# Kernel tuning notes

Hardware: AMD Instinct MI355X
Metric: run time of the kernel (lower is better)

Reference implementation:

```python
import jax, jax.numpy as jnp
import numpy as np

EMB = 512
GP = 128
NH = 8
HD = EMB // NH  # 64
B = 2
S = 1024


def _rel_shift(x):
    # Faithful port of DoubleAttentionLayer._rel_shift (pads dim 1, reinterprets
    # (B, J+1, K, n) as (J+1, B, K, n), drops first slice). Row-major reshape
    # semantics match torch .view on contiguous tensors exactly.
    Bsz, J, K, N = x.shape
    zp = jnp.zeros((Bsz, 1, K, N), x.dtype)
    xp = jnp.concatenate([zp, x], axis=1).reshape(J + 1, Bsz, K, N)
    return xp[1:].reshape(Bsz, J, K, N)


def _layernorm(x):
    # nn.LayerNorm(emb_dim, elementwise_affine=False), eps=1e-5
    m = jnp.mean(x, axis=-1, keepdims=True)
    v = jnp.var(x, axis=-1, keepdims=True)
    return (x - m) / jnp.sqrt(v + 1e-5)


def _attention(q, k, v, Bc, Bp, gpe, mask, Wp_w, Wp_b):
    Bsz, J, E = q.shape
    K = k.shape[1]
    # content scores
    qc = jnp.tanh((q + Bc).reshape(Bsz, J, NH, HD))
    kh = jnp.tanh(k.reshape(Bsz, K, NH, HD))
    ctx = jnp.einsum('bjnd,bknd->bjkn', qc, kh)
    # position scores (tanh before reshape in source for qp -- elementwise, same math)
    qp = jnp.tanh(q + Bp).reshape(Bsz, J, NH, HD)
    kp = jnp.tanh((gpe @ Wp_w + Wp_b).reshape(Bsz, -1, NH, HD))
    pos = jnp.einsum('bjnd,bknd->bjkn', qp, kp)
    pad = ctx.shape[2] - pos.shape[2]  # static; 0 in this configuration
    if pad > 0:
        # replicate-pad pos at front of k dim; constant(0)-pad mask (torch F.pad defaults)
        pos = jnp.concatenate([jnp.broadcast_to(pos[:, :, :1], (Bsz, J, pad, NH)), pos], axis=2)
        mask = jnp.concatenate([jnp.zeros(mask.shape[:2] + (pad, mask.shape[3]), mask.dtype), mask], axis=2)
    pos = _rel_shift(pos)
    att = (ctx + pos) / (HD ** 0.5) - 1e30 * mask
    att = jax.nn.softmax(att, axis=2)
    vh = jnp.tanh(v.reshape(Bsz, K, NH, HD))
    return jnp.einsum('bjkn,bknd->bjnd', att, vh).reshape(Bsz, J, E)


def setup_inputs() -> dict:
    key = jax.random.key(0)
    ks = jax.random.split(key, 12)
    u_emb = jax.random.normal(ks[0], (B, S, EMB), jnp.float32)
    f_emb = jax.random.normal(ks[1], (B, S, EMB), jnp.float32)
    gpe = jax.random.normal(ks[2], (B, S, GP), jnp.float32)
    # causal masks: 1 where attention is disallowed, broadcast over heads
    causal = (1.0 - jnp.tril(jnp.ones((S, S), jnp.float32)))[None, :, :, None]
    u_mask = jnp.broadcast_to(causal, (B, S, S, 1))
    f_mask = jnp.broadcast_to(causal, (B, S, S, 1))
    w = 0.02
    Wq_w = w * jax.random.normal(ks[3], (EMB, EMB), jnp.float32)
    Wq_b = jnp.zeros((EMB,), jnp.float32)
    Wkv_w = w * jax.random.normal(ks[4], (EMB, 2 * EMB), jnp.float32)
    Wkv_b = jnp.zeros((2 * EMB,), jnp.float32)
    Wp_w = w * jax.random.normal(ks[5], (GP, EMB), jnp.float32)
    Wp_b = jnp.zeros((EMB,), jnp.float32)
    Wu_w = w * jax.random.normal(ks[6], (EMB, EMB), jnp.float32)
    Wu_b = jnp.zeros((EMB,), jnp.float32)
    Bfc = 0.2 * jax.random.normal(ks[7], (1, 1, EMB), jnp.float32)
    Bfp = 0.2 * jax.random.normal(ks[8], (1, 1, EMB), jnp.float32)
    Buc = 0.2 * jax.random.normal(ks[9], (1, 1, EMB), jnp.float32)
    Bup = 0.2 * jax.random.normal(ks[10], (1, 1, EMB), jnp.float32)
    return {"u_emb": u_emb, "f_emb": f_emb, "gpe": gpe, "u_mask": u_mask, "f_mask": f_mask,
            "Wq_w": Wq_w, "Wq_b": Wq_b, "Wkv_w": Wkv_w, "Wkv_b": Wkv_b,
            "Wp_w": Wp_w, "Wp_b": Wp_b, "Wu_w": Wu_w, "Wu_b": Wu_b,
            "Bfc": Bfc, "Bfp": Bfp, "Buc": Buc, "Bup": Bup}


def reference(u_emb, f_emb, gpe, u_mask, f_mask, Wq_w, Wq_b, Wkv_w, Wkv_b,
              Wp_w, Wp_b, Wu_w, Wu_b, Bfc, Bfp, Buc, Bup):
    # first_part=True path: f_mem = f_emb (memory buffer registration has no output effect)
    q_u = f_emb @ Wu_w + Wu_b
    kv = f_emb @ Wkv_w + Wkv_b
    k, v = jnp.split(kv, 2, axis=-1)
    u_out = _layernorm(u_emb + _attention(q_u, k, v, Buc, Bup, gpe, u_mask, Wp_w, Wp_b))
    # last_layer=False: second attention over f stream
    q_f = f_emb @ Wq_w + Wq_b
    f_out = _layernorm(f_emb + _attention(q_f, k, v, Bfc, Bfp, gpe, f_mask, Wp_w, Wp_b))
    return (u_out, f_out)
```

## Files before the change

### kernel.cpp

```cpp
#include <hip/hip_runtime.h>
#include <math.h>

#define EMB 512
#define NH 8
#define HD 64
#define BB 2
#define SS 1024
#define ROWS (BB * SS)

typedef __attribute__((ext_vector_type(8))) short bhalf8;
typedef __attribute__((ext_vector_type(4))) float f32x4;
typedef __attribute__((ext_vector_type(8))) unsigned short us8;
typedef unsigned short ushort_t;

typedef const __attribute__((address_space(1))) void gas_void;
typedef __attribute__((address_space(3))) void las_void;

__device__ __forceinline__ void gl2lds16(const void* g, void* l) {
  __builtin_amdgcn_global_load_lds((gas_void*)g, (las_void*)l, 16, 0, 0);
}

__device__ __forceinline__ unsigned short f2bf(float x) {
  unsigned u = __float_as_uint(x);
  u = (u + 0x7FFFu + ((u >> 16) & 1u)) >> 16;
  return (unsigned short)u;
}
__device__ __forceinline__ float bf2f(unsigned short v) {
  return __uint_as_float(((unsigned)v) << 16);
}
__device__ __forceinline__ float fast_tanh(float x) {
  x = fminf(15.f, fmaxf(-15.f, x));
  const float e = __expf(2.f * x);
  return (e - 1.f) / (e + 1.f);
}

__global__ __launch_bounds__(256, 4) void projpe_kernel(
    const float* __restrict__ f_emb, const float* __restrict__ gpe,
    const float* __restrict__ Wu, const float* __restrict__ Wq,
    const float* __restrict__ Wkv, const float* __restrict__ Wp,
    const float* __restrict__ Wu_b, const float* __restrict__ Wq_b,
    const float* __restrict__ Wkv_b, const float* __restrict__ Wp_b,
    const float* __restrict__ Buc, const float* __restrict__ Bup,
    const float* __restrict__ Bfc, const float* __restrict__ Bfp,
    ushort_t* __restrict__ Qcomb, ushort_t* __restrict__ Kcomb,
    ushort_t* __restrict__ vhT, float* __restrict__ Onum,
    float* __restrict__ lpart) {
  const int bx = blockIdx.x;
  const int mb = blockIdx.y * 128;
  const int tid = threadIdx.x;
  const int w = tid >> 6, lane = tid & 63;
  const int ln = lane & 15, quad = lane >> 4;
  const int wm = (w >> 1) * 64, wn = (w & 1) * 32;

  __shared__ __align__(16) ushort_t sA[128 * 72];
  __shared__ __align__(16) ushort_t sB[64 * 72];

  const int fb = blockIdx.y * 40 + bx;
  if (fb < 512) {
    const float4 z4 = {0.f, 0.f, 0.f, 0.f};
#pragma unroll
    for (int i = 0; i < 4; ++i)
      ((float4*)Onum)[(size_t)fb * 1024 + i * 256 + tid] = z4;
  } else {
    lpart[(fb - 512) * 256 + tid] = 0.f;
  }
  if (fb == 0) {
    const int t2 = tid >> 7, rem = tid & 127;
    const int h = rem >> 4, d4 = (rem & 15) * 4;
    *(ushort4*)&Qcomb[((size_t)t2 * ROWS + 1023) * 1024 + h * 128 + 64 + d4] =
        make_ushort4(0, 0, 0, 0);
  }

  const bool isPe = (bx >= 32);
  const int nb = isPe ? 0 : bx * 64;
  const int npbase = isPe ? (bx - 32) * 64 : 0;
  const float* Af = isPe ? gpe : f_emb;
  const int lda = isPe ? 128 : 512;
  const int trips = isPe ? 2 : 8;

  const float* Wsrc;
  int Nw, coff;
  if (isPe) { Wsrc = Wp; Nw = 512; coff = npbase; }
  else if (nb < 512) { Wsrc = Wu; Nw = 512; coff = nb; }
  else if (nb < 1024) { Wsrc = Wq; Nw = 512; coff = nb - 512; }
  else { Wsrc = Wkv; Nw = 1024; coff = nb - 1024; }

  const int bn = tid & 63;
  const int bk0 = (tid >> 6) * 16;

  f32x4 acc[4][2];
#pragma unroll
  for (int rt = 0; rt < 4; ++rt)
#pragma unroll
    for (int ct = 0; ct < 2; ++ct) acc[rt][ct] = (f32x4){0.f, 0.f, 0.f, 0.f};

  float4 qa[8];
  float qbw[16];
#pragma unroll
  for (int i = 0; i < 4; ++i) {
    const int idx = tid + i * 256;
    const size_t base = (size_t)(mb + (idx >> 3)) * lda + (idx & 7) * 8;
    qa[2 * i] = *(const float4*)&Af[base];
    qa[2 * i + 1] = *(const float4*)&Af[base + 4];
  }
#pragma unroll
  for (int j = 0; j < 16; ++j)
    qbw[j] = Wsrc[(size_t)(bk0 + j) * Nw + coff + bn];

  for (int t0 = 0; t0 < trips; ++t0) {
    __syncthreads();
#pragma unroll
    for (int i = 0; i < 4; ++i) {
      const int idx = tid + i * 256;
      us8 o;
      const float4 a = qa[2 * i], b = qa[2 * i + 1];
      o[0] = f2bf(a.x); o[1] = f2bf(a.y); o[2] = f2bf(a.z); o[3] = f2bf(a.w);
      o[4] = f2bf(b.x); o[5] = f2bf(b.y); o[6] = f2bf(b.z); o[7] = f2bf(b.w);
      *(us8*)&sA[(idx >> 3) * 72 + (idx & 7) * 8] = o;
    }
    {
      us8 o0, o1;
#pragma unroll
      for (int j = 0; j < 8; ++j) {
        o0[j] = f2bf(qbw[j]);
        o1[j] = f2bf(qbw[8 + j]);
      }
      *(us8*)&sB[bn * 72 + bk0] = o0;
      *(us8*)&sB[bn * 72 + bk0 + 8] = o1;
    }
    __syncthreads();
    if (t0 < trips - 1) {
      const int k1 = (t0 + 1) * 64;
#pragma unroll
      for (int i = 0; i < 4; ++i) {
        const int idx = tid + i * 256;
        const size_t base = (size_t)(mb + (idx >> 3)) * lda + k1 + (idx & 7) * 8;
        qa[2 * i] = *(const float4*)&Af[base];
        qa[2 * i + 1] = *(const float4*)&Af[base + 4];
      }
#pragma unroll
      for (int j = 0; j < 16; ++j)
        qbw[j] = Wsrc[(size_t)(k1 + bk0 + j) * Nw + coff + bn];
    }
#pragma unroll
    for (int kc = 0; kc < 2; ++kc) {
      bhalf8 af[4], bf_[2];
#pragma unroll
      for (int rt = 0; rt < 4; ++rt)
        af[rt] =
            *(const bhalf8*)&sA[(wm + rt * 16 + ln) * 72 + kc * 32 + quad * 8];
#pragma unroll
      for (int ct = 0; ct < 2; ++ct)
        bf_[ct] =
            *(const bhalf8*)&sB[(wn + ct * 16 + ln) * 72 + kc * 32 + quad * 8];
#pragma unroll
      for (int rt = 0; rt < 4; ++rt)
#pragma unroll
        for (int ct = 0; ct < 2; ++ct)
          acc[rt][ct] = __builtin_amdgcn_mfma_f32_16x16x32_bf16(
              af[rt], bf_[ct], acc[rt][ct], 0, 0, 0);
    }
  }

  __syncthreads();
  ushort_t* sOut = sA;

  if (!isPe && nb >= 1536) {
#pragma unroll
    for (int ct = 0; ct < 2; ++ct) {
      const int nl = wn + ct * 16 + ln;
      const float wb = Wkv_b[nb + nl - 1024];
#pragma unroll
      for (int rt = 0; rt < 4; ++rt)
#pragma unroll
        for (int r = 0; r < 4; ++r) {
          const int ml = wm + rt * 16 + quad * 4 + r;
          sOut[nl * 136 + ml] = f2bf(fast_tanh(acc[rt][ct][r] + wb));
        }
    }
    __syncthreads();
    const int b = mb >> 10, mo = mb & 1023;
#pragma unroll
    for (int i = 0; i < 4; ++i) {
      const int idx = tid + i * 256;
      const int nl = idx >> 4, m8 = (idx & 15) * 8;
      const us8 v = *(const us8*)&sOut[nl * 136 + m8];
      *(us8*)&vhT[((size_t)b * 512 + (nb - 1536) + nl) * 1024 + mo + m8] = v;
    }
  } else {
    const float* WB =
        isPe ? Wp_b : (nb < 512 ? Wu_b : (nb < 1024 ? Wq_b : Wkv_b));
    const int woff =
        isPe ? npbase : (nb < 512 ? nb : (nb < 1024 ? nb - 512 : nb - 1024));
    const bool rawDump = (!isPe && nb < 1024);
#pragma unroll
    for (int ct = 0; ct < 2; ++ct) {
      const int nl = wn + ct * 16 + ln;
      const float wb = WB[woff + nl];
#pragma unroll
      for (int rt = 0; rt < 4; ++rt)
#pragma unroll
        for (int r = 0; r < 4; ++r) {
          const int ml = wm + rt * 16 + quad * 4 + r;
          const float v = acc[rt][ct][r] + wb;
          sOut[ml * 72 + nl] = f2bf(rawDump ? v : fast_tanh(v));
        }
    }
    __syncthreads();
#pragma unroll
    for (int i = 0; i < 4; ++i) {
      const int idx = tid + i * 256;
      const int rr = idx >> 3, c8 = (idx & 7) * 8;
      const int m = mb + rr;
      const us8 v = *(const us8*)&sOut[rr * 72 + c8];
      if (isPe) {
        const int n = npbase + c8;
        const int h = n >> 6;
        *(us8*)&Kcomb[(size_t)m * 1024 + h * 128 + 64 + (n & 63)] = v;
      } else if (nb < 1024) {
        const int strm = nb >= 512 ? 1 : 0;
        const int n = (nb - strm * 512) + c8;
        const int h = n >> 6;
        const float* BC = strm ? Bfc : Buc;
        const float* BP = strm ? Bfp : Bup;
        float bcA[8], bpA[8];
        *(float4*)&bcA[0] = *(const float4*)&BC[n];
        *(float4*)&bcA[4] = *(const float4*)&BC[n + 4];
        *(float4*)&bpA[0] = *(const float4*)&BP[n];
        *(float4*)&bpA[4] = *(const float4*)&BP[n + 4];
        us8 oc, op;
#pragma unroll
        for (int jj = 0; jj < 8; ++jj) {
          const float vv = bf2f((unsigned short)v[jj]);
          oc[jj] = f2bf(fast_tanh(vv + bcA[jj]));
          op[jj] = f2bf(fast_tanh(vv + bpA[jj]));
        }
        *(us8*)&Qcomb[((size_t)strm * ROWS + m) * 1024 + h * 128 + (n & 63)] =
            oc;
        if (m != 0) {
          const int mp = (m < 1024) ? m - 1 : m;
          *(us8*)&Qcomb[((size_t)strm * ROWS + mp) * 1024 + h * 128 + 64 +
                        (n & 63)] = op;
        }
      } else {
        const int n = (nb - 1024) + c8;
        const int h = n >> 6;
        *(us8*)&Kcomb[(size_t)m * 1024 + h * 128 + (n & 63)] = v;
      }
    }
  }
}

__global__ __launch_bounds__(256, 2) void attn_kernel(
    const ushort_t* __restrict__ Qcomb, const ushort_t* __restrict__ Kcomb,
    const ushort_t* __restrict__ vhT, float* __restrict__ Onum,
    float* __restrict__ lpart) {
  const int bid = blockIdx.x;
  const int tid = threadIdx.x;
  const int w = tid >> 6, lane = tid & 63;
  const int ln = lane & 15, quad = lane >> 4;

  __shared__ __align__(16) ushort_t sK[2 * 64 * 128];
  __shared__ __align__(16) ushort_t sV[2 * 64 * 64];
  __shared__ __align__(16) ushort_t sP[64 * 72];

  const int G0 = (bid * 17) >> 1;
  const int G1 = ((bid + 1) * 17) >> 1;
  const int cnt = G1 - G0;

  int c = G0 / 136;
  int u = G0 - c * 136;
  int jt = (int)((sqrtf(8.f * u + 1.f) - 1.f) * 0.5f);
  while ((jt + 1) * (jt + 2) / 2 <= u) ++jt;
  while (jt * (jt + 1) / 2 > u) --jt;
  int kt = u - jt * (jt + 1) / 2;
  int t = c >> 4, b = (c >> 3) & 1, h = c & 7;

  const int l4 = lane >> 4, p15 = lane & 15;
  const int l3 = lane >> 3, l7 = lane & 7;
#define STAGE_KV(B_, H_, KT_, BUF_)                                          \
  {                                                                          \
    const size_t kb_ = ((size_t)(B_)*SS + (KT_)*64) * 1024 + (H_)*128;       \
    ushort_t* bk_ = sK + (BUF_)*8192;                                        \
    _Pragma("unroll") for (int s_ = 0; s_ < 4; ++s_) {                       \
      const int q_ = w * 4 + s_;                                             \
      const int r_ = q_ * 4 + l4;                                            \
      const int gl_ = p15 ^ (r_ & 7);                                        \
      gl2lds16(&Kcomb[kb_ + (size_t)r_ * 1024 + gl_ * 8], &bk_[q_ * 512]);   \
    }                                                                        \
    const size_t vb_ = ((size_t)(B_)*512 + (H_)*64) * 1024 + (KT_)*64;       \
    ushort_t* bv_ = sV + (BUF_)*4096;                                        \
    _Pragma("unroll") for (int s_ = 0; s_ < 2; ++s_) {                       \
      const int q_ = w * 2 + s_;                                             \
      const int r_ = q_ * 8 + l3;                                            \
      const int gl_ = l7 ^ (r_ & 7);                                         \
      gl2lds16(&vhT[vb_ + (size_t)r_ * 1024 + gl_ * 8], &bv_[q_ * 512]);     \
    }                                                                        \
  }

  bhalf8 aq[4];
#define LOAD_AQ(T_, B_, H_, JT_)                                             \
  {                                                                          \
    const size_t qb_ =                                                       \
        ((size_t)(T_)*ROWS + (B_)*SS + (JT_)*64 + w * 16 + ln) * 1024 +      \
        (H_)*128 + quad * 8;                                                 \
    _Pragma("unroll") for (int kc_ = 0; kc_ < 4; ++kc_) aq[kc_] =            \
        *(const bhalf8*)&Qcomb[qb_ + kc_ * 32];                              \
  }

  STAGE_KV(b, h, kt, 0);
  LOAD_AQ(t, b, h, jt);

  f32x4 oacc[4];
#pragma unroll
  for (int ct = 0; ct < 4; ++ct) oacc[ct] = (f32x4){0.f, 0.f, 0.f, 0.f};
  float lsum[4] = {0.f, 0.f, 0.f, 0.f};

  for (int it = 0; it < cnt; ++it) {
    __syncthreads();
    const ushort_t* bK = sK + (it & 1) * 8192;
    const ushort_t* bV = sV + (it & 1) * 4096;

    int c2 = c, jt2 = jt, kt2 = kt + 1;
    if (kt2 > jt) {
      jt2 = jt + 1; kt2 = 0;
      if (jt2 > 15) { c2 = c + 1; jt2 = 0; }
    }
    if (it < cnt - 1) {
      const int b2 = (c2 >> 3) & 1, h2 = c2 & 7;
      STAGE_KV(b2, h2, kt2, ((it + 1) & 1));
    }

    f32x4 sacc[4];
#pragma unroll
    for (int ct = 0; ct < 4; ++ct) {
      sacc[ct] = (f32x4){0.f, 0.f, 0.f, 0.f};
#pragma unroll
      for (int kc = 0; kc < 4; ++kc) {
        const bhalf8 bk = *(const bhalf8*)&bK[(ct * 16 + ln) * 128 +
                                             (((kc * 4 + quad) ^ l7) << 3)];
        sacc[ct] = __builtin_amdgcn_mfma_f32_16x16x32_bf16(aq[kc], bk,
                                                           sacc[ct], 0, 0, 0);
      }
    }

    const bool diag = (kt == jt);
#pragma unroll
    for (int ct = 0; ct < 4; ++ct)
#pragma unroll
      for (int r = 0; r < 4; ++r) {
        float p;
        if (diag && (ct * 16 + ln > w * 16 + quad * 4 + r))
          p = 0.f;
        else
          p = __expf(sacc[ct][r] * 0.125f - 16.f);
        sacc[ct][r] = p;
        lsum[r] += p;
      }

#pragma unroll
    for (int ct = 0; ct < 4; ++ct)
#pragma unroll
      for (int r = 0; r < 4; ++r)
        sP[(w * 16 + quad * 4 + r) * 72 + ct * 16 + ln] =
            (ushort_t)(__float_as_uint(sacc[ct][r]) >> 16);

#pragma unroll
    for (int kc = 0; kc < 2; ++kc) {
      const bhalf8 ap =
          *(const bhalf8*)&sP[(w * 16 + ln) * 72 + kc * 32 + quad * 8];
#pragma unroll
      for (int ct = 0; ct < 4; ++ct) {
        const bhalf8 bv = *(const bhalf8*)&bV[(ct * 16 + ln) * 64 +
                                             (((kc * 4 + quad) ^ l7) << 3)];
        oacc[ct] = __builtin_amdgcn_mfma_f32_16x16x32_bf16(ap, bv, oacc[ct],
                                                           0, 0, 0);
      }
    }

    const bool rowEnd = (it == cnt - 1) || (jt2 != jt) || (c2 != c);
    if (rowEnd) {
#pragma unroll
      for (int r = 0; r < 4; ++r) {
        float s = lsum[r];
        s += __shfl_xor(s, 1);
        s += __shfl_xor(s, 2);
        s += __shfl_xor(s, 4);
        s += __shfl_xor(s, 8);
        const int j = jt * 64 + w * 16 + quad * 4 + r;
        if (ln == 0)
          atomicAdd(&lpart[((((t * 2 + b) << 10) + j) << 3) + h], s);
        const size_t orow = (((size_t)t * ROWS + b * SS + j) << 9) + h * 64;
#pragma unroll
        for (int ct = 0; ct < 4; ++ct)
          atomicAdd(&Onum[orow + ct * 16 + ln], oacc[ct][r]);
        lsum[r] = 0.f;
      }
#pragma unroll
      for (int ct = 0; ct < 4; ++ct) oacc[ct] = (f32x4){0.f, 0.f, 0.f, 0.f};
      if (it < cnt - 1) {
        const int t2 = c2 >> 4, b2 = (c2 >> 3) & 1, h2 = c2 & 7;
        LOAD_AQ(t2, b2, h2, jt2);
      }
    }
    c = c2; jt = jt2; kt = kt2;
    t = c >> 4; b = (c >> 3) & 1; h = c & 7;
  }
}

__global__ __launch_bounds__(256) void ln_kernel(
    const float* __restrict__ u_emb, const float* __restrict__ f_emb,
    const float* __restrict__ Onum, const float* __restrict__ lpart,
    float* __restrict__ out) {
  const int rid = blockIdx.x * 4 + (threadIdx.x >> 6);
  const int lane = threadIdx.x & 63;
  const int t = rid >> 11, row = rid & 2047;
  const int b = row >> 10, j = row & 1023;
  const float* resid = t ? f_emb : u_emb;
  const size_t base = (size_t)row * 512;
  const size_t obase = ((size_t)t * ROWS + row) * 512;
  const int o = lane * 8;
  const int h = lane >> 3;
  const float inv = 1.f / lpart[((((t * 2 + b) << 10) + j) << 3) + h];

  const float4 n0 = *(const float4*)&Onum[obase + o];
  const float4 n1 = *(const float4*)&Onum[obase + o + 4];
  const float4 r0 = *(const float4*)&resid[base + o];
  const float4 r1 = *(const float4*)&resid[base + o + 4];
  float y[8];
  y[0] = r0.x + n0.x * inv; y[1] = r0.y + n0.y * inv;
  y[2] = r0.z + n0.z * inv; y[3] = r0.w + n0.w * inv;
  y[4] = r1.x + n1.x * inv; y[5] = r1.y + n1.y * inv;
  y[6] = r1.z + n1.z * inv; y[7] = r1.w + n1.w * inv;

  float s = 0.f, q = 0.f;
#pragma unroll
  for (int i = 0; i < 8; ++i) {
    s += y[i];
    q += y[i] * y[i];
  }
#pragma unroll
  for (int off = 1; off < 64; off <<= 1) {
    s += __shfl_xor(s, off);
    q += __shfl_xor(q, off);
  }
  const float mean = s * (1.f / 512.f);
  const float var = q * (1.f / 512.f) - mean * mean;
  const float rstd = rsqrtf(var + 1e-5f);

  float4 o0, o1;
  o0.x = (y[0] - mean) * rstd; o0.y = (y[1] - mean) * rstd;
  o0.z = (y[2] - mean) * rstd; o0.w = (y[3] - mean) * rstd;
  o1.x = (y[4] - mean) * rstd; o1.y = (y[5] - mean) * rstd;
  o1.z = (y[6] - mean) * rstd; o1.w = (y[7] - mean) * rstd;
  *(float4*)&out[obase + o] = o0;
  *(float4*)&out[obase + o + 4] = o1;
}

extern "C" void kernel_launch(void* const* d_in, const int* in_sizes, int n_in,
                              void* d_out, int out_size, void* d_ws,
                              size_t ws_size, hipStream_t stream) {
  (void)in_sizes; (void)n_in; (void)out_size; (void)ws_size;
  const float* u_emb = (const float*)d_in[0];
  const float* f_emb = (const float*)d_in[1];
  const float* gpe = (const float*)d_in[2];
  const float* Wq_w = (const float*)d_in[5];
  const float* Wq_b = (const float*)d_in[6];
  const float* Wkv_w = (const float*)d_in[7];
  const float* Wkv_b = (const float*)d_in[8];
  const float* Wp_w = (const float*)d_in[9];
  const float* Wp_b = (const float*)d_in[10];
  const float* Wu_w = (const float*)d_in[11];
  const float* Wu_b = (const float*)d_in[12];
  const float* Bfc = (const float*)d_in[13];
  const float* Bfp = (const float*)d_in[14];
  const float* Buc = (const float*)d_in[15];
  const float* Bup = (const float*)d_in[16];
  float* out = (float*)d_out;

  ushort_t* ws = (ushort_t*)d_ws;
  const size_t SZ = (size_t)ROWS * EMB;
  ushort_t* Qcomb = ws;
  ushort_t* Kcomb = ws + 4 * SZ;
  ushort_t* vhT = ws + 6 * SZ;
  float* Onum = (float*)(ws + 7 * SZ);
  float* lpart = (float*)(ws + 11 * SZ);

  dim3 blk(256);
  hipLaunchKernelGGL(projpe_kernel, dim3(40, 16), blk, 0, stream, f_emb, gpe,
                     Wu_w, Wq_w, Wkv_w, Wp_w, Wu_b, Wq_b, Wkv_b, Wp_b, Buc,
                     Bup, Bfc, Bfp, Qcomb, Kcomb, vhT, Onum, lpart);
  hipLaunchKernelGGL(attn_kernel, dim3(512), blk, 0, stream, Qcomb, Kcomb, vhT,
                     Onum, lpart);
  hipLaunchKernelGGL(ln_kernel, dim3(1024), blk, 0, stream, u_emb, f_emb, Onum,
                     lpart, out);
}
```

Measured before the change: 158.2 us.

## Replace atomic accumulation with per-tile partials reduced in layernorm kernel

Attention work is now split so each block owns a K tile (paired z and 15-z for balance) and walks query tiles. Instead of atomically adding into a zeroed fp32 numerator, each block writes bf16 partial output tiles and fp32 row sums to per-slot buffers. The layernorm kernel then sums those partials over key tiles. This drops the atomics, the zeroing pass and the double buffering, and raises occupancy. In exchange it adds bf16 rounding of the partials, more global traffic in the reduction, and no prefetch overlap.

```diff
diff --git a/kernel.cpp b/kernel.cpp
--- a/kernel.cpp
+++ b/kernel.cpp
@@ -43,8 +43,7 @@
     const float* __restrict__ Buc, const float* __restrict__ Bup,
     const float* __restrict__ Bfc, const float* __restrict__ Bfp,
     ushort_t* __restrict__ Qcomb, ushort_t* __restrict__ Kcomb,
-    ushort_t* __restrict__ vhT, float* __restrict__ Onum,
-    float* __restrict__ lpart) {
+    ushort_t* __restrict__ vhT) {
   const int bx = blockIdx.x;
   const int mb = blockIdx.y * 128;
   const int tid = threadIdx.x;
@@ -55,16 +54,7 @@
   __shared__ __align__(16) ushort_t sA[128 * 72];
   __shared__ __align__(16) ushort_t sB[64 * 72];
 
-  const int fb = blockIdx.y * 40 + bx;
-  if (fb < 512) {
-    const float4 z4 = {0.f, 0.f, 0.f, 0.f};
-#pragma unroll
-    for (int i = 0; i < 4; ++i)
-      ((float4*)Onum)[(size_t)fb * 1024 + i * 256 + tid] = z4;
-  } else {
-    lpart[(fb - 512) * 256 + tid] = 0.f;
-  }
-  if (fb == 0) {
+  if (bx == 0 && blockIdx.y == 0) {
     const int t2 = tid >> 7, rem = tid & 127;
     const int h = rem >> 4, d4 = (rem & 15) * 4;
     *(ushort4*)&Qcomb[((size_t)t2 * ROWS + 1023) * 1024 + h * 128 + 64 + d4] =
@@ -251,135 +241,115 @@
   }
 }
 
-__global__ __launch_bounds__(256, 2) void attn_kernel(
+__global__ __launch_bounds__(256, 4) void attn_kernel(
     const ushort_t* __restrict__ Qcomb, const ushort_t* __restrict__ Kcomb,
-    const ushort_t* __restrict__ vhT, float* __restrict__ Onum,
-    float* __restrict__ lpart) {
+    const ushort_t* __restrict__ vhT, ushort_t* __restrict__ Opart,
+    float* __restrict__ Lpart) {
   const int bid = blockIdx.x;
   const int tid = threadIdx.x;
   const int w = tid >> 6, lane = tid & 63;
   const int ln = lane & 15, quad = lane >> 4;
 
-  __shared__ __align__(16) ushort_t sK[2 * 64 * 128];
-  __shared__ __align__(16) ushort_t sV[2 * 64 * 64];
+  __shared__ __align__(16) ushort_t sK[64 * 128];
+  __shared__ __align__(16) ushort_t sV[64 * 64];
   __shared__ __align__(16) ushort_t sP[64 * 72];
 
-  const int G0 = (bid * 17) >> 1;
-  const int G1 = ((bid + 1) * 17) >> 1;
-  const int cnt = G1 - G0;
-
-  int c = G0 / 136;
-  int u = G0 - c * 136;
-  int jt = (int)((sqrtf(8.f * u + 1.f) - 1.f) * 0.5f);
-  while ((jt + 1) * (jt + 2) / 2 <= u) ++jt;
-  while (jt * (jt + 1) / 2 > u) --jt;
-  int kt = u - jt * (jt + 1) / 2;
-  int t = c >> 4, b = (c >> 3) & 1, h = c & 7;
+  const int c = bid & 31;
+  const int z = (bid >> 5) & 7;
+  const int q = bid >> 8;
+  const int t = c >> 4, b = (c >> 3) & 1, h = c & 7;
 
   const int l4 = lane >> 4, p15 = lane & 15;
   const int l3 = lane >> 3, l7 = lane & 7;
-#define STAGE_KV(B_, H_, KT_, BUF_)                                          \
+
+#define STAGE_KV(B_, H_, KT_)                                                \
   {                                                                          \
     const size_t kb_ = ((size_t)(B_)*SS + (KT_)*64) * 1024 + (H_)*128;       \
-    ushort_t* bk_ = sK + (BUF_)*8192;                                        \
     _Pragma("unroll") for (int s_ = 0; s_ < 4; ++s_) {                       \
       const int q_ = w * 4 + s_;                                             \
       const int r_ = q_ * 4 + l4;                                            \
       const int gl_ = p15 ^ (r_ & 7);                                        \
-      gl2lds16(&Kcomb[kb_ + (size_t)r_ * 1024 + gl_ * 8], &bk_[q_ * 512]);   \
+      gl2lds16(&Kcomb[kb_ + (size_t)r_ * 1024 + gl_ * 8], &sK[q_ * 512]);    \
     }                                                                        \
     const size_t vb_ = ((size_t)(B_)*512 + (H_)*64) * 1024 + (KT_)*64;       \
-    ushort_t* bv_ = sV + (BUF_)*4096;                                        \
     _Pragma("unroll") for (int s_ = 0; s_ < 2; ++s_) {                       \
       const int q_ = w * 2 + s_;                                             \
       const int r_ = q_ * 8 + l3;                                            \
       const int gl_ = l7 ^ (r_ & 7);                                         \
-      gl2lds16(&vhT[vb_ + (size_t)r_ * 1024 + gl_ * 8], &bv_[q_ * 512]);     \
+      gl2lds16(&vhT[vb_ + (size_t)r_ * 1024 + gl_ * 8], &sV[q_ * 512]);      \
     }                                                                        \
   }
 
-  bhalf8 aq[4];
-#define LOAD_AQ(T_, B_, H_, JT_)                                             \
-  {                                                                          \
-    const size_t qb_ =                                                       \
-        ((size_t)(T_)*ROWS + (B_)*SS + (JT_)*64 + w * 16 + ln) * 1024 +      \
-        (H_)*128 + quad * 8;                                                 \
-    _Pragma("unroll") for (int kc_ = 0; kc_ < 4; ++kc_) aq[kc_] =            \
-        *(const bhalf8*)&Qcomb[qb_ + kc_ * 32];                              \
-  }
-
-  STAGE_KV(b, h, kt, 0);
-  LOAD_AQ(t, b, h, jt);
-
-  f32x4 oacc[4];
-#pragma unroll
-  for (int ct = 0; ct < 4; ++ct) oacc[ct] = (f32x4){0.f, 0.f, 0.f, 0.f};
-  float lsum[4] = {0.f, 0.f, 0.f, 0.f};
-
-  for (int it = 0; it < cnt; ++it) {
+#pragma unroll
+  for (int col = 0; col < 2; ++col) {
+    const int kt = col ? (15 - z) : z;
+    if (col) __syncthreads();
+    STAGE_KV(b, h, kt);
     __syncthreads();
-    const ushort_t* bK = sK + (it & 1) * 8192;
-    const ushort_t* bV = sV + (it & 1) * 4096;
-
-    int c2 = c, jt2 = jt, kt2 = kt + 1;
-    if (kt2 > jt) {
-      jt2 = jt + 1; kt2 = 0;
-      if (jt2 > 15) { c2 = c + 1; jt2 = 0; }
-    }
-    if (it < cnt - 1) {
-      const int b2 = (c2 >> 3) & 1, h2 = c2 & 7;
-      STAGE_KV(b2, h2, kt2, ((it + 1) & 1));
-    }
-
-    f32x4 sacc[4];
-#pragma unroll
-    for (int ct = 0; ct < 4; ++ct) {
-      sacc[ct] = (f32x4){0.f, 0.f, 0.f, 0.f};
-#pragma unroll
-      for (int kc = 0; kc < 4; ++kc) {
-        const bhalf8 bk = *(const bhalf8*)&bK[(ct * 16 + ln) * 128 +
-                                             (((kc * 4 + quad) ^ l7) << 3)];
-        sacc[ct] = __builtin_amdgcn_mfma_f32_16x16x32_bf16(aq[kc], bk,
-                                                           sacc[ct], 0, 0, 0);
-      }
-    }
-
-    const bool diag = (kt == jt);
-#pragma unroll
-    for (int ct = 0; ct < 4; ++ct)
-#pragma unroll
-      for (int r = 0; r < 4; ++r) {
-        float p;
-        if (diag && (ct * 16 + ln > w * 16 + quad * 4 + r))
-          p = 0.f;
-        else
-          p = __expf(sacc[ct][r] * 0.125f - 16.f);
-        sacc[ct][r] = p;
-        lsum[r] += p;
-      }
-
-#pragma unroll
-    for (int ct = 0; ct < 4; ++ct)
-#pragma unroll
-      for (int r = 0; r < 4; ++r)
-        sP[(w * 16 + quad * 4 + r) * 72 + ct * 16 + ln] =
-            (ushort_t)(__float_as_uint(sacc[ct][r]) >> 16);
-
-#pragma unroll
-    for (int kc = 0; kc < 2; ++kc) {
-      const bhalf8 ap =
-          *(const bhalf8*)&sP[(w * 16 + ln) * 72 + kc * 32 + quad * 8];
+
+    for (int jt = kt + q; jt <= 15; jt += 4) {
+      bhalf8 aq[4];
+      {
+        const size_t qb = ((size_t)t * ROWS + b * SS + jt * 64 + w * 16 + ln) *
+                              1024 + h * 128 + quad * 8;
+#pragma unroll
+        for (int kc = 0; kc < 4; ++kc)
+          aq[kc] = *(const bhalf8*)&Qcomb[qb + kc * 32];
+      }
+
+      f32x4 sacc[4];
 #pragma unroll
       for (int ct = 0; ct < 4; ++ct) {
-        const bhalf8 bv = *(const bhalf8*)&bV[(ct * 16 + ln) * 64 +
-                                             (((kc * 4 + quad) ^ l7) << 3)];
-        oacc[ct] = __builtin_amdgcn_mfma_f32_16x16x32_bf16(ap, bv, oacc[ct],
-                                                           0, 0, 0);
-      }
-    }
-
-    const bool rowEnd = (it == cnt - 1) || (jt2 != jt) || (c2 != c);
-    if (rowEnd) {
+        sacc[ct] = (f32x4){0.f, 0.f, 0.f, 0.f};
+#pragma unroll
+        for (int kc = 0; kc < 4; ++kc) {
+          const bhalf8 bk = *(const bhalf8*)&sK[(ct * 16 + ln) * 128 +
+                                               (((kc * 4 + quad) ^ l7) << 3)];
+          sacc[ct] = __builtin_amdgcn_mfma_f32_16x16x32_bf16(aq[kc], bk,
+                                                             sacc[ct], 0, 0, 0);
+        }
+      }
+
+      const bool diag = (jt == kt);
+      float lsum[4] = {0.f, 0.f, 0.f, 0.f};
+#pragma unroll
+      for (int ct = 0; ct < 4; ++ct)
+#pragma unroll
+        for (int r = 0; r < 4; ++r) {
+          float p;
+          if (diag && (ct * 16 + ln > w * 16 + quad * 4 + r))
+            p = 0.f;
+          else
+            p = __expf(sacc[ct][r] * 0.125f - 16.f);
+          sacc[ct][r] = p;
+          lsum[r] += p;
+        }
+
+#pragma unroll
+      for (int ct = 0; ct < 4; ++ct)
+#pragma unroll
+        for (int r = 0; r < 4; ++r)
+          sP[(w * 16 + quad * 4 + r) * 72 + ct * 16 + ln] =
+              (ushort_t)(__float_as_uint(sacc[ct][r]) >> 16);
+
+      f32x4 oacc[4];
+#pragma unroll
+      for (int ct = 0; ct < 4; ++ct) oacc[ct] = (f32x4){0.f, 0.f, 0.f, 0.f};
+#pragma unroll
+      for (int kc = 0; kc < 2; ++kc) {
+        const bhalf8 ap =
+            *(const bhalf8*)&sP[(w * 16 + ln) * 72 + kc * 32 + quad * 8];
+#pragma unroll
+        for (int ct = 0; ct < 4; ++ct) {
+          const bhalf8 bv = *(const bhalf8*)&sV[(ct * 16 + ln) * 64 +
+                                               (((kc * 4 + quad) ^ l7) << 3)];
+          oacc[ct] = __builtin_amdgcn_mfma_f32_16x16x32_bf16(ap, bv, oacc[ct],
+                                                             0, 0, 0);
+        }
+      }
+
+      const int slot = c * 136 + (jt * (jt + 1)) / 2 + kt;
+
 #pragma unroll
       for (int r = 0; r < 4; ++r) {
         float s = lsum[r];
@@ -387,65 +357,76 @@
         s += __shfl_xor(s, 2);
         s += __shfl_xor(s, 4);
         s += __shfl_xor(s, 8);
-        const int j = jt * 64 + w * 16 + quad * 4 + r;
         if (ln == 0)
-          atomicAdd(&lpart[((((t * 2 + b) << 10) + j) << 3) + h], s);
-        const size_t orow = (((size_t)t * ROWS + b * SS + j) << 9) + h * 64;
-#pragma unroll
-        for (int ct = 0; ct < 4; ++ct)
-          atomicAdd(&Onum[orow + ct * 16 + ln], oacc[ct][r]);
-        lsum[r] = 0.f;
-      }
-#pragma unroll
-      for (int ct = 0; ct < 4; ++ct) oacc[ct] = (f32x4){0.f, 0.f, 0.f, 0.f};
-      if (it < cnt - 1) {
-        const int t2 = c2 >> 4, b2 = (c2 >> 3) & 1, h2 = c2 & 7;
-        LOAD_AQ(t2, b2, h2, jt2);
-      }
-    }
-    c = c2; jt = jt2; kt = kt2;
-    t = c >> 4; b = (c >> 3) & 1; h = c & 7;
+          Lpart[(size_t)slot * 64 + w * 16 + quad * 4 + r] = s;
+      }
+
+#pragma unroll
+      for (int ct = 0; ct < 4; ++ct)
+#pragma unroll
+        for (int r = 0; r < 4; ++r)
+          sP[(w * 16 + quad * 4 + r) * 72 + ct * 16 + ln] = f2bf(oacc[ct][r]);
+      {
+        const int rr = lane >> 2, cc = (lane & 3) * 16;
+        const us8 v0 = *(const us8*)&sP[(w * 16 + rr) * 72 + cc];
+        const us8 v1 = *(const us8*)&sP[(w * 16 + rr) * 72 + cc + 8];
+        const size_t obase = (size_t)slot * 4096 + (w * 16 + rr) * 64 + cc;
+        *(us8*)&Opart[obase] = v0;
+        *(us8*)&Opart[obase + 8] = v1;
+      }
+    }
   }
 }
 
 __global__ __launch_bounds__(256) void ln_kernel(
     const float* __restrict__ u_emb, const float* __restrict__ f_emb,
-    const float* __restrict__ Onum, const float* __restrict__ lpart,
+    const ushort_t* __restrict__ Opart, const float* __restrict__ Lpart,
     float* __restrict__ out) {
   const int rid = blockIdx.x * 4 + (threadIdx.x >> 6);
   const int lane = threadIdx.x & 63;
   const int t = rid >> 11, row = rid & 2047;
   const int b = row >> 10, j = row & 1023;
+  const int jt = j >> 6, jr = j & 63;
   const float* resid = t ? f_emb : u_emb;
   const size_t base = (size_t)row * 512;
   const size_t obase = ((size_t)t * ROWS + row) * 512;
   const int o = lane * 8;
-  const int h = lane >> 3;
-  const float inv = 1.f / lpart[((((t * 2 + b) << 10) + j) << 3) + h];
-
-  const float4 n0 = *(const float4*)&Onum[obase + o];
-  const float4 n1 = *(const float4*)&Onum[obase + o + 4];
+  const int h = lane >> 3, d8 = o & 63;
+  const int c = t * 16 + b * 8 + h;
+  const int slot0 = c * 136 + (jt * (jt + 1)) / 2;
+
+  float acc[8] = {0.f, 0.f, 0.f, 0.f, 0.f, 0.f, 0.f, 0.f};
+  float l = 0.f;
+  for (int kt = 0; kt <= jt; ++kt) {
+    const us8 v =
+        *(const us8*)&Opart[(size_t)(slot0 + kt) * 4096 + jr * 64 + d8];
+#pragma unroll
+    for (int i = 0; i < 8; ++i) acc[i] += bf2f((unsigned short)v[i]);
+    l += Lpart[(size_t)(slot0 + kt) * 64 + jr];
+  }
+  const float inv = 1.f / l;
+
   const float4 r0 = *(const float4*)&resid[base + o];
   const float4 r1 = *(const float4*)&resid[base + o + 4];
   float y[8];
-  y[0] = r0.x + n0.x * inv; y[1] = r0.y + n0.y * inv;
-  y[2] = r0.z + n0.z * inv; y[3] = r0.w + n0.w * inv;
-  y[4] = r1.x + n1.x * inv; y[5] = r1.y + n1.y * inv;
-  y[6] = r1.z + n1.z * inv; y[7] = r1.w + n1.w * inv;
-
-  float s = 0.f, q = 0.f;
+  y[0] = r0.x + acc[0] * inv; y[1] = r0.y + acc[1] * inv;
+  y[2] = r0.z + acc[2] * inv; y[3] = r0.w + acc[3] * inv;
+  y[4] = r1.x + acc[4] * inv; y[5] = r1.y + acc[5] * inv;
+  y[6] = r1.z + acc[6] * inv; y[7] = r1.w + acc[7] * inv;
+
+  float s = 0.f, qq = 0.f;
 #pragma unroll
   for (int i = 0; i < 8; ++i) {
     s += y[i];
-    q += y[i] * y[i];
+    qq += y[i] * y[i];
   }
 #pragma unroll
   for (int off = 1; off < 64; off <<= 1) {
     s += __shfl_xor(s, off);
-    q += __shfl_xor(q, off);
+    qq += __shfl_xor(qq, off);
   }
   const float mean = s * (1.f / 512.f);
-  const float var = q * (1.f / 512.f) - mean * mean;
+  const float var = qq * (1.f / 512.f) - mean * mean;
   const float rstd = rsqrtf(var + 1e-5f);
 
   float4 o0, o1;
@@ -483,15 +464,15 @@
   ushort_t* Qcomb = ws;
   ushort_t* Kcomb = ws + 4 * SZ;
   ushort_t* vhT = ws + 6 * SZ;
-  float* Onum = (float*)(ws + 7 * SZ);
-  float* lpart = (float*)(ws + 11 * SZ);
+  ushort_t* Opart = ws + 7 * SZ;
+  float* Lpart = (float*)(ws + 7 * SZ + 17825792);
 
   dim3 blk(256);
   hipLaunchKernelGGL(projpe_kernel, dim3(40, 16), blk, 0, stream, f_emb, gpe,
                      Wu_w, Wq_w, Wkv_w, Wp_w, Wu_b, Wq_b, Wkv_b, Wp_b, Buc,
-                     Bup, Bfc, Bfp, Qcomb, Kcomb, vhT, Onum, lpart);
-  hipLaunchKernelGGL(attn_kernel, dim3(512), blk, 0, stream, Qcomb, Kcomb, vhT,
-                     Onum, lpart);
-  hipLaunchKernelGGL(ln_kernel, dim3(1024), blk, 0, stream, u_emb, f_emb, Onum,
-                     lpart, out);
-}
+                     Bup, Bfc, Bfp, Qcomb, Kcomb, vhT);
+  hipLaunchKernelGGL(attn_kernel, dim3(1024), blk, 0, stream, Qcomb, Kcomb,
+                     vhT, Opart, Lpart);
+  hipLaunchKernelGGL(ln_kernel, dim3(1024), blk, 0, stream, u_emb, f_emb,
+                     Opart, Lpart, out);
+}
```

Result: slower. 195.3 us (+23.5%).

## Alias P scratch into spare V buffer to fit three blocks per CU

Applied to the files above, without the earlier changes.

The separate P scratch buffer is removed. Each wave now writes its softmax probabilities into the idle half of the double-buffered V staging area, using an XOR-swizzled layout instead of a padded one. Staging of the next V tile moves to after the PV MFMAs, behind a sched_barrier. This cuts shared memory per block so the launch bound can be raised to three blocks per CU for more latency hiding. The cost is less overlap for the V prefetch, and correctness relies on each wave's P rows coinciding with the V rows that same wave stages.

```diff
diff --git a/kernel.cpp b/kernel.cpp
--- a/kernel.cpp
+++ b/kernel.cpp
@@ -251,7 +251,7 @@
   }
 }
 
-__global__ __launch_bounds__(256, 2) void attn_kernel(
+__global__ __launch_bounds__(256, 3) void attn_kernel(
     const ushort_t* __restrict__ Qcomb, const ushort_t* __restrict__ Kcomb,
     const ushort_t* __restrict__ vhT, float* __restrict__ Onum,
     float* __restrict__ lpart) {
@@ -261,8 +261,7 @@
   const int ln = lane & 15, quad = lane >> 4;
 
   __shared__ __align__(16) ushort_t sK[2 * 64 * 128];
-  __shared__ __align__(16) ushort_t sV[2 * 64 * 64];
-  __shared__ __align__(16) ushort_t sP[64 * 72];
+  __shared__ __align__(16) ushort_t sPV[2 * 64 * 64];
 
   const int G0 = (bid * 17) >> 1;
   const int G1 = ((bid + 1) * 17) >> 1;
@@ -278,7 +277,8 @@
 
   const int l4 = lane >> 4, p15 = lane & 15;
   const int l3 = lane >> 3, l7 = lane & 7;
-#define STAGE_KV(B_, H_, KT_, BUF_)                                          \
+
+#define STAGE_K(B_, H_, KT_, BUF_)                                           \
   {                                                                          \
     const size_t kb_ = ((size_t)(B_)*SS + (KT_)*64) * 1024 + (H_)*128;       \
     ushort_t* bk_ = sK + (BUF_)*8192;                                        \
@@ -288,8 +288,11 @@
       const int gl_ = p15 ^ (r_ & 7);                                        \
       gl2lds16(&Kcomb[kb_ + (size_t)r_ * 1024 + gl_ * 8], &bk_[q_ * 512]);   \
     }                                                                        \
+  }
+#define STAGE_V(B_, H_, KT_, BUF_)                                           \
+  {                                                                          \
     const size_t vb_ = ((size_t)(B_)*512 + (H_)*64) * 1024 + (KT_)*64;       \
-    ushort_t* bv_ = sV + (BUF_)*4096;                                        \
+    ushort_t* bv_ = sPV + (BUF_)*4096;                                       \
     _Pragma("unroll") for (int s_ = 0; s_ < 2; ++s_) {                       \
       const int q_ = w * 2 + s_;                                             \
       const int r_ = q_ * 8 + l3;                                            \
@@ -308,7 +311,8 @@
         *(const bhalf8*)&Qcomb[qb_ + kc_ * 32];                              \
   }
 
-  STAGE_KV(b, h, kt, 0);
+  STAGE_K(b, h, kt, 0);
+  STAGE_V(b, h, kt, 0);
   LOAD_AQ(t, b, h, jt);
 
   f32x4 oacc[4];
@@ -319,17 +323,16 @@
   for (int it = 0; it < cnt; ++it) {
     __syncthreads();
     const ushort_t* bK = sK + (it & 1) * 8192;
-    const ushort_t* bV = sV + (it & 1) * 4096;
+    const ushort_t* bV = sPV + (it & 1) * 4096;
+    ushort_t* pscr = sPV + ((it + 1) & 1) * 4096;
 
     int c2 = c, jt2 = jt, kt2 = kt + 1;
     if (kt2 > jt) {
       jt2 = jt + 1; kt2 = 0;
       if (jt2 > 15) { c2 = c + 1; jt2 = 0; }
     }
-    if (it < cnt - 1) {
-      const int b2 = (c2 >> 3) & 1, h2 = c2 & 7;
-      STAGE_KV(b2, h2, kt2, ((it + 1) & 1));
-    }
+    const int b2 = (c2 >> 3) & 1, h2 = c2 & 7;
+    if (it < cnt - 1) STAGE_K(b2, h2, kt2, ((it + 1) & 1));
 
     f32x4 sacc[4];
 #pragma unroll
@@ -361,22 +364,28 @@
 #pragma unroll
     for (int ct = 0; ct < 4; ++ct)
 #pragma unroll
-      for (int r = 0; r < 4; ++r)
-        sP[(w * 16 + quad * 4 + r) * 72 + ct * 16 + ln] =
+      for (int r = 0; r < 4; ++r) {
+        const int pr = w * 16 + quad * 4 + r;
+        const int pg = ((ct * 2 + (ln >> 3)) ^ (pr & 7)) << 3;
+        pscr[pr * 64 + pg + (ln & 7)] =
             (ushort_t)(__float_as_uint(sacc[ct][r]) >> 16);
+      }
 
 #pragma unroll
     for (int kc = 0; kc < 2; ++kc) {
-      const bhalf8 ap =
-          *(const bhalf8*)&sP[(w * 16 + ln) * 72 + kc * 32 + quad * 8];
+      const bhalf8 ap = *(const bhalf8*)&pscr[(w * 16 + ln) * 64 +
+                                             (((kc * 4 + quad) ^ l7) << 3)];
 #pragma unroll
       for (int ct = 0; ct < 4; ++ct) {
         const bhalf8 bv = *(const bhalf8*)&bV[(ct * 16 + ln) * 64 +
                                              (((kc * 4 + quad) ^ l7) << 3)];
-        oacc[ct] = __builtin_amdgcn_mfma_f32_16x16x32_bf16(ap, bv, oacc[ct],
-                                                           0, 0, 0);
-      }
-    }
+        oacc[ct] =
+            __builtin_amdgcn_mfma_f32_16x16x32_bf16(ap, bv, oacc[ct], 0, 0, 0);
+      }
+    }
+
+    __builtin_amdgcn_sched_barrier(0);
+    if (it < cnt - 1) STAGE_V(b2, h2, kt2, ((it + 1) & 1));
 
     const bool rowEnd = (it == cnt - 1) || (jt2 != jt) || (c2 != c);
     if (rowEnd) {
@@ -399,7 +408,7 @@
 #pragma unroll
       for (int ct = 0; ct < 4; ++ct) oacc[ct] = (f32x4){0.f, 0.f, 0.f, 0.f};
       if (it < cnt - 1) {
-        const int t2 = c2 >> 4, b2 = (c2 >> 3) & 1, h2 = c2 & 7;
+        const int t2 = c2 >> 4;
         LOAD_AQ(t2, b2, h2, jt2);
       }
     }
```

Measured after the change: 158.8 us. Within noise of the previous version (+0.4%).
